# Performance work log

Hardware: AMD Instinct MI355X
Metric: run time of the kernel (lower is better)

The kernel has to match this reference:

```python
import jax, jax.numpy as jnp
import numpy as np

NUM_NODES = 51681
EMBED_DIM = 32
HIDDEN_DIM = 64
NUM_EDGES = 2048  # input_dim == edge_weight.size(0)


def gcn_conv(x, W, b, src, dst, edge_weight, num_nodes):
    """PyG GCNConv with add_self_loops=True, symmetric normalization.
    x: [N, Fin], W: [Fin, Fout], b: [Fout], src/dst: [E], edge_weight: [E].
    """
    loop = jnp.arange(num_nodes)
    row = jnp.concatenate([src, loop])            # source of message
    col = jnp.concatenate([dst, loop])            # target (aggregation) node
    w = jnp.concatenate([edge_weight, jnp.ones((num_nodes,), x.dtype)])
    deg = jax.ops.segment_sum(w, col, num_segments=num_nodes)   # [N]
    dinv = jnp.where(deg > 0, jax.lax.rsqrt(deg), 0.0)
    norm = dinv[row] * w * dinv[col]              # [E+N]
    xw = x @ W                                    # [N, Fout]
    msgs = norm[:, None] * xw[row]                # gather + scale
    out = jax.ops.segment_sum(msgs, col, num_segments=num_nodes)
    return out + b


def setup_inputs() -> dict:
    key = jax.random.key(0)
    ks = jax.random.split(key, 12)
    edge_index = jax.random.randint(ks[0], (2, NUM_EDGES), 0, NUM_NODES)
    edge_weight = jax.random.uniform(ks[1], (NUM_EDGES,), dtype=jnp.float32)
    embedding = jax.random.normal(ks[2], (NUM_NODES, EMBED_DIM), jnp.float32)
    def lin(k, fin, fout):
        return jax.random.normal(k, (fin, fout), jnp.float32) / np.sqrt(fin)
    return {
        "edge_index": edge_index,
        "edge_weight": edge_weight,
        "embedding": embedding,
        "enc_W1": lin(ks[3], EMBED_DIM, HIDDEN_DIM),
        "enc_b1": jnp.zeros((HIDDEN_DIM,), jnp.float32),
        "enc_W2": lin(ks[4], HIDDEN_DIM, EMBED_DIM),
        "enc_b2": jnp.zeros((EMBED_DIM,), jnp.float32),
        "dec_W1": lin(ks[5], EMBED_DIM, HIDDEN_DIM),
        "dec_b1": jnp.zeros((HIDDEN_DIM,), jnp.float32),
        "dec_W2": lin(ks[6], HIDDEN_DIM, NUM_EDGES),
        "dec_b2": jnp.zeros((NUM_EDGES,), jnp.float32),
    }


def reference(edge_index, edge_weight, embedding,
              enc_W1, enc_b1, enc_W2, enc_b2,
              dec_W1, dec_b1, dec_W2, dec_b2):
    src, dst = edge_index[0], edge_index[1]
    # Encoder
    x = jax.nn.relu(gcn_conv(embedding, enc_W1, enc_b1, src, dst, edge_weight, NUM_NODES))
    z = jax.nn.relu(gcn_conv(x, enc_W2, enc_b2, src, dst, edge_weight, NUM_NODES))
    # Decoder
    h = jax.nn.relu(gcn_conv(z, dec_W1, dec_b1, src, dst, edge_weight, NUM_NODES))
    recon_x = gcn_conv(h, dec_W2, dec_b2, src, dst, edge_weight, NUM_NODES)
    return recon_x, z
```

## Files before the change

### kernel.cpp

```cpp
#include <hip/hip_runtime.h>

#define NN 51681
#define EE 2048
#define Z_OFF (51681LL * 2048LL)

typedef __bf16 bf16x8 __attribute__((ext_vector_type(8)));
typedef unsigned short ushort8 __attribute__((ext_vector_type(8)));
typedef float floatx4 __attribute__((ext_vector_type(4)));

__device__ inline unsigned short f2bf(float x) {
    unsigned u = __float_as_uint(x);
    unsigned r = (u + 0x7FFFu + ((u >> 16) & 1u)) >> 16;
    return (unsigned short)r;
}
__device__ inline float bf2f(unsigned short h) {
    return __uint_as_float(((unsigned)h) << 16);
}


__global__ void init_k(const float* __restrict__ W4,
                       ushort* __restrict__ wthi, ushort* __restrict__ wtlo,
                       float* __restrict__ deg, const int* __restrict__ dst,
                       float* __restrict__ E1, float* __restrict__ E2,
                       float* __restrict__ E3, float* __restrict__ E4) {
    int b = blockIdx.x, t = threadIdx.x;
    if (b < 512) {
        int i = b * 256 + t;
        int k = i >> 11, c = i & 2047;
        float x = W4[i];
        ushort h = f2bf(x);
        ushort l = f2bf(x - bf2f(h));
        wthi[c * 64 + k] = h;
        wtlo[c * 64 + k] = l;
    } else if (b < 714) {
        int i = (b - 512) * 256 + t;
        if (i < NN) deg[i] = 1.0f;
    } else {
        int j = (b - 714) * 256 + t;
        float4 zz = make_float4(0.f, 0.f, 0.f, 0.f);
        if (j < 16384) {
            int e = j >> 3, f = j & 7;
            reinterpret_cast<float4*>(&E1[(long long)dst[e] * 32])[f] = zz;
        } else if (j < 49152) {
            int jj = j - 16384; int e = jj >> 4, f = jj & 15;
            reinterpret_cast<float4*>(&E2[(long long)dst[e] * 64])[f] = zz;
        } else if (j < 65536) {
            int jj = j - 49152; int e = jj >> 3, f = jj & 7;
            reinterpret_cast<float4*>(&E3[(long long)dst[e] * 32])[f] = zz;
        } else if (j < 98304) {
            int jj = j - 65536; int e = jj >> 4, f = jj & 15;
            reinterpret_cast<float4*>(&E4[(long long)dst[e] * 64])[f] = zz;
        }
    }
}

__global__ void deg_scatter_k(const int* __restrict__ dst, const float* __restrict__ w,
                              float* __restrict__ deg) {
    int e = blockIdx.x * 256 + threadIdx.x;
    if (e < EE) atomicAdd(&deg[dst[e]], w[e]);
}


template<int FIN>
__global__ void edge_scatter_k(const int* __restrict__ src, const int* __restrict__ dst,
                               const float* __restrict__ ew, const float* __restrict__ deg,
                               const float* __restrict__ X, float* __restrict__ E) {
    constexpr int F4 = FIN / 4;
    int tid = blockIdx.x * 256 + threadIdx.x;
    if (tid >= EE * F4) return;
    int e = tid / F4;
    int f = (tid - e * F4) * 4;
    int s = src[e], d = dst[e];
    float n = rsqrtf(deg[s]) * ew[e] * rsqrtf(deg[d]);
    const float4 v = *reinterpret_cast<const float4*>(&X[(long long)s * FIN + f]);
    float* a = &E[(long long)d * FIN + f];
    atomicAdd(a + 0, n * v.x);
    atomicAdd(a + 1, n * v.y);
    atomicAdd(a + 2, n * v.z);
    atomicAdd(a + 3, n * v.w);
}


template<int K, int FOUT, bool RELU>
__global__ __launch_bounds__(256) void gemm_small_k(
    const float* __restrict__ E, const float* __restrict__ X,
    const float* __restrict__ deg, const float* __restrict__ W,
    const float* __restrict__ bias, float* __restrict__ out) {
    constexpr int NPB = 256 / FOUT;
    __shared__ float Ws[K * FOUT];
    __shared__ float As[NPB][K];
    __shared__ float bs[FOUT];
    int tid = threadIdx.x;
    for (int i = tid; i < K * FOUT / 4; i += 256)
        reinterpret_cast<float4*>(Ws)[i] = reinterpret_cast<const float4*>(W)[i];
    if (tid < FOUT) bs[tid] = bias[tid];
    int node0 = blockIdx.x * NPB;
    for (int i = tid; i < NPB * (K / 4); i += 256) {
        int r = i / (K / 4);
        int kk = (i - r * (K / 4)) * 4;
        int g = node0 + r;
        float4 v = make_float4(0.f, 0.f, 0.f, 0.f);
        if (g < NN) {
            float dg = deg[g];
            float s = 1.0f / dg;
            float4 xv = *reinterpret_cast<const float4*>(&X[(long long)g * K + kk]);
            v = make_float4(xv.x * s, xv.y * s, xv.z * s, xv.w * s);
            if (dg != 1.0f) {
                float4 ev = *reinterpret_cast<const float4*>(&E[(long long)g * K + kk]);
                v.x += ev.x; v.y += ev.y; v.z += ev.z; v.w += ev.w;
            }
        }
        *reinterpret_cast<float4*>(&As[r][kk]) = v;
    }
    __syncthreads();
    int ln = tid / FOUT;
    int n  = tid - ln * FOUT;
    int g = node0 + ln;
    if (g >= NN) return;
    float s = bs[n];
    #pragma unroll
    for (int k = 0; k < K; ++k)
        s = fmaf(As[ln][k], Ws[k * FOUT + n], s);
    if (RELU) s = fmaxf(s, 0.f);
    out[(long long)g * FOUT + n] = s;
}


__global__ __launch_bounds__(512, 4) void gemm_big_k(
    const float* __restrict__ E, const float* __restrict__ H,
    const float* __restrict__ deg,
    const ushort* __restrict__ wthi, const ushort* __restrict__ wtlo,
    const float* __restrict__ bias, float* __restrict__ out) {
    __shared__ ushort Whi[128 * 64];
    __shared__ ushort Wlo[128 * 64];
    int tid  = threadIdx.x;
    int lane = tid & 63;
    int wv   = tid >> 6;
    int rl   = lane & 15;
    int kg   = lane >> 4;
    int cbase = blockIdx.x * 128;
    int node  = blockIdx.y * 128 + wv * 16 + rl;
    bool valid = node < NN;

    {
        const ushort8* sh = reinterpret_cast<const ushort8*>(wthi + (size_t)cbase * 64);
        const ushort8* sl = reinterpret_cast<const ushort8*>(wtlo + (size_t)cbase * 64);
        #pragma unroll
        for (int i = tid; i < 1024; i += 512) {
            int col = i >> 3, slot = i & 7;
            int d = col * 8 + (slot ^ (col & 7));
            reinterpret_cast<ushort8*>(Whi)[d] = sh[i];
            reinterpret_cast<ushort8*>(Wlo)[d] = sl[i];
        }
    }

    floatx4 bv[8];
    #pragma unroll
    for (int tl = 0; tl < 8; ++tl)
        bv[tl] = *reinterpret_cast<const floatx4*>(&bias[cbase + tl * 16 + kg * 4]);

    bf16x8 nb_hi[2], nb_lo[2];
    {
        float v[2][8];
        if (valid) {
            float dg = deg[node];
            float s = 1.0f / dg;
            const float* h0 = H + (long long)node * 64 + kg * 8;
            #pragma unroll
            for (int f = 0; f < 2; ++f) {
                float4 ha = *reinterpret_cast<const float4*>(h0 + f * 32);
                float4 hb = *reinterpret_cast<const float4*>(h0 + f * 32 + 4);
                v[f][0] = ha.x * s; v[f][1] = ha.y * s; v[f][2] = ha.z * s; v[f][3] = ha.w * s;
                v[f][4] = hb.x * s; v[f][5] = hb.y * s; v[f][6] = hb.z * s; v[f][7] = hb.w * s;
            }
            if (dg != 1.0f) {
                const float* e0 = E + (long long)node * 64 + kg * 8;
                #pragma unroll
                for (int f = 0; f < 2; ++f) {
                    float4 ea = *reinterpret_cast<const float4*>(e0 + f * 32);
                    float4 eb = *reinterpret_cast<const float4*>(e0 + f * 32 + 4);
                    v[f][0] += ea.x; v[f][1] += ea.y; v[f][2] += ea.z; v[f][3] += ea.w;
                    v[f][4] += eb.x; v[f][5] += eb.y; v[f][6] += eb.z; v[f][7] += eb.w;
                }
            }
        } else {
            #pragma unroll
            for (int f = 0; f < 2; ++f)
                #pragma unroll
                for (int i = 0; i < 8; ++i) v[f][i] = 0.f;
        }
        #pragma unroll
        for (int f = 0; f < 2; ++f) {
            ushort8 h8, l8;
            #pragma unroll
            for (int i = 0; i < 8; ++i) {
                unsigned u = __float_as_uint(v[f][i]) & 0xFFFF0000u;
                h8[i] = (unsigned short)(u >> 16);
                l8[i] = f2bf(v[f][i] - __uint_as_float(u));
            }
            nb_hi[f] = __builtin_bit_cast(bf16x8, h8);
            nb_lo[f] = __builtin_bit_cast(bf16x8, l8);
        }
    }

    __syncthreads();

    long long obase = (long long)node * 2048 + cbase + kg * 4;
    #pragma unroll
    for (int tl = 0; tl < 8; ++tl) {
        int col  = tl * 16 + rl;
        int base = col * 64;
        int s0 = (kg ^ (rl & 7)) * 8;
        int s1 = ((kg + 4) ^ (rl & 7)) * 8;
        bf16x8 wh0 = *reinterpret_cast<const bf16x8*>(&Whi[base + s0]);
        bf16x8 wh1 = *reinterpret_cast<const bf16x8*>(&Whi[base + s1]);
        bf16x8 wl0 = *reinterpret_cast<const bf16x8*>(&Wlo[base + s0]);
        bf16x8 wl1 = *reinterpret_cast<const bf16x8*>(&Wlo[base + s1]);

        floatx4 acc = bv[tl];
        acc = __builtin_amdgcn_mfma_f32_16x16x32_bf16(wh0, nb_hi[0], acc, 0, 0, 0);
        acc = __builtin_amdgcn_mfma_f32_16x16x32_bf16(wh0, nb_lo[0], acc, 0, 0, 0);
        acc = __builtin_amdgcn_mfma_f32_16x16x32_bf16(wl0, nb_hi[0], acc, 0, 0, 0);
        acc = __builtin_amdgcn_mfma_f32_16x16x32_bf16(wh1, nb_hi[1], acc, 0, 0, 0);
        acc = __builtin_amdgcn_mfma_f32_16x16x32_bf16(wh1, nb_lo[1], acc, 0, 0, 0);
        acc = __builtin_amdgcn_mfma_f32_16x16x32_bf16(wl1, nb_hi[1], acc, 0, 0, 0);

        if (valid)
            *reinterpret_cast<floatx4*>(&out[obase + tl * 16]) = acc;
    }
}


extern "C" void kernel_launch(void* const* d_in, const int* in_sizes, int n_in,
                              void* d_out, int out_size, void* d_ws, size_t ws_size,
                              hipStream_t stream) {
    const int*   edge_index = (const int*)d_in[0];
    const int*   src = edge_index;
    const int*   dst = edge_index + EE;
    const float* ew  = (const float*)d_in[1];
    const float* emb = (const float*)d_in[2];
    const float* W1  = (const float*)d_in[3];
    const float* b1  = (const float*)d_in[4];
    const float* W2  = (const float*)d_in[5];
    const float* b2  = (const float*)d_in[6];
    const float* W3  = (const float*)d_in[7];
    const float* b3  = (const float*)d_in[8];
    const float* W4  = (const float*)d_in[9];
    const float* b4  = (const float*)d_in[10];

    float* out = (float*)d_out;
    float* z   = out + Z_OFF;

    float* ws   = (float*)d_ws;
    float* deg  = ws;
    float* E1   = ws + 51712;
    float* E2   = E1 + 1653792;
    float* E3   = E2 + 3307584;
    float* E4   = E3 + 1653792;
    float* t1   = E4 + 3307584;
    ushort* wthi = (ushort*)(t1 + 3307584);
    ushort* wtlo = wthi + 131072;

    init_k<<<1098, 256, 0, stream>>>(W4, wthi, wtlo, deg, dst, E1, E2, E3, E4);
    deg_scatter_k<<<(EE + 255) / 256, 256, 0, stream>>>(dst, ew, deg);

    edge_scatter_k<32><<<(EE * 8 + 255) / 256, 256, 0, stream>>>(src, dst, ew, deg, emb, E1);
    gemm_small_k<32, 64, true><<<(NN + 3) / 4, 256, 0, stream>>>(E1, emb, deg, W1, b1, t1);

    edge_scatter_k<64><<<(EE * 16 + 255) / 256, 256, 0, stream>>>(src, dst, ew, deg, t1, E2);
    gemm_small_k<64, 32, true><<<(NN + 7) / 8, 256, 0, stream>>>(E2, t1, deg, W2, b2, z);

    edge_scatter_k<32><<<(EE * 8 + 255) / 256, 256, 0, stream>>>(src, dst, ew, deg, z, E3);
    gemm_small_k<32, 64, true><<<(NN + 3) / 4, 256, 0, stream>>>(E3, z, deg, W3, b3, t1);

    edge_scatter_k<64><<<(EE * 16 + 255) / 256, 256, 0, stream>>>(src, dst, ew, deg, t1, E4);
    gemm_big_k<<<dim3(16, 404), 512, 0, stream>>>(E4, t1, deg, wthi, wtlo, b4, out);
}
```

Before: 184.0 us.

## Fold degree computation into init kernel and remap big GEMM block order

Removes the separate degree scatter launch. Each node now computes its degree in the init kernel by scanning all edges held in shared memory, replacing the atomics and one kernel launch with brute-force per-node work. The big GEMM also remaps block indices so that consecutive blocks cover different row strips and column tiles, which may change cache locality for the output writes and the weight tiles.

```diff
diff --git a/kernel.cpp b/kernel.cpp
--- a/kernel.cpp
+++ b/kernel.cpp
@@ -18,11 +18,13 @@
 }
 
 
-__global__ void init_k(const float* __restrict__ W4,
-                       ushort* __restrict__ wthi, ushort* __restrict__ wtlo,
-                       float* __restrict__ deg, const int* __restrict__ dst,
-                       float* __restrict__ E1, float* __restrict__ E2,
-                       float* __restrict__ E3, float* __restrict__ E4) {
+__global__ __launch_bounds__(256) void init_k(
+    const float* __restrict__ W4, const int* __restrict__ dst,
+    const float* __restrict__ ew,
+    ushort* __restrict__ wthi, ushort* __restrict__ wtlo,
+    float* __restrict__ deg,
+    float* __restrict__ E1, float* __restrict__ E2,
+    float* __restrict__ E3, float* __restrict__ E4) {
     int b = blockIdx.x, t = threadIdx.x;
     if (b < 512) {
         int i = b * 256 + t;
@@ -33,8 +35,16 @@
         wthi[c * 64 + k] = h;
         wtlo[c * 64 + k] = l;
     } else if (b < 714) {
-        int i = (b - 512) * 256 + t;
-        if (i < NN) deg[i] = 1.0f;
+        __shared__ int   sdst[EE];
+        __shared__ float swt[EE];
+        for (int i = t; i < EE; i += 256) { sdst[i] = dst[i]; swt[i] = ew[i]; }
+        __syncthreads();
+        int node = (b - 512) * 256 + t;
+        float d = 1.0f;
+        #pragma unroll 8
+        for (int e = 0; e < EE; ++e)
+            d += (sdst[e] == node) ? swt[e] : 0.0f;
+        if (node < NN) deg[node] = d;
     } else {
         int j = (b - 714) * 256 + t;
         float4 zz = make_float4(0.f, 0.f, 0.f, 0.f);
@@ -52,12 +62,6 @@
             reinterpret_cast<float4*>(&E4[(long long)dst[e] * 64])[f] = zz;
         }
     }
-}
-
-__global__ void deg_scatter_k(const int* __restrict__ dst, const float* __restrict__ w,
-                              float* __restrict__ deg) {
-    int e = blockIdx.x * 256 + threadIdx.x;
-    if (e < EE) atomicAdd(&deg[dst[e]], w[e]);
 }
 
 
@@ -138,19 +142,25 @@
     int wv   = tid >> 6;
     int rl   = lane & 15;
     int kg   = lane >> 4;
-    int cbase = blockIdx.x * 128;
-    int node  = blockIdx.y * 128 + wv * 16 + rl;
+
+    int lin  = blockIdx.x + 16 * blockIdx.y;
+    int nlin = (lin & 7) * 808 + (lin >> 3);
+    int bx   = nlin & 15;
+    int by   = nlin >> 4;
+
+    int cbase = bx * 128;
+    int node  = by * 128 + wv * 16 + rl;
     bool valid = node < NN;
 
     {
-        const ushort8* sh = reinterpret_cast<const ushort8*>(wthi + (size_t)cbase * 64);
-        const ushort8* sl = reinterpret_cast<const ushort8*>(wtlo + (size_t)cbase * 64);
+        const ushort8* sh8 = reinterpret_cast<const ushort8*>(wthi + (size_t)cbase * 64);
+        const ushort8* sl8 = reinterpret_cast<const ushort8*>(wtlo + (size_t)cbase * 64);
         #pragma unroll
         for (int i = tid; i < 1024; i += 512) {
             int col = i >> 3, slot = i & 7;
             int d = col * 8 + (slot ^ (col & 7));
-            reinterpret_cast<ushort8*>(Whi)[d] = sh[i];
-            reinterpret_cast<ushort8*>(Wlo)[d] = sl[i];
+            reinterpret_cast<ushort8*>(Whi)[d] = sh8[i];
+            reinterpret_cast<ushort8*>(Wlo)[d] = sl8[i];
         }
     }
 
@@ -261,8 +271,7 @@
     ushort* wthi = (ushort*)(t1 + 3307584);
     ushort* wtlo = wthi + 131072;
 
-    init_k<<<1098, 256, 0, stream>>>(W4, wthi, wtlo, deg, dst, E1, E2, E3, E4);
-    deg_scatter_k<<<(EE + 255) / 256, 256, 0, stream>>>(dst, ew, deg);
+    init_k<<<1098, 256, 0, stream>>>(W4, dst, ew, wthi, wtlo, deg, E1, E2, E3, E4);
 
     edge_scatter_k<32><<<(EE * 8 + 255) / 256, 256, 0, stream>>>(src, dst, ew, deg, emb, E1);
     gemm_small_k<32, 64, true><<<(NN + 3) / 4, 256, 0, stream>>>(E1, emb, deg, W1, b1, t1);
```

Result: slower. 282.4 us (+53.5%).
